# Kernel tuning notes

Measured on AMD Instinct MI355X. Metric: run time of the kernel, lower is better.

The kernel has to match this reference:

```python
import jax, jax.numpy as jnp
import numpy as np

C_M = 256   # norm_channel (msa channel)
C_Z = 128   # pair_channel
H = 8       # num_head
C = 32      # attention_channel per head


def layer_norm(x, gamma, beta, eps=1e-5):
    mu = jnp.mean(x, axis=-1, keepdims=True)
    var = jnp.var(x, axis=-1, keepdims=True)
    return (x - mu) * jax.lax.rsqrt(var + eps) * gamma + beta


def setup_inputs() -> dict:
    key = jax.random.key(0)
    ks = jax.random.split(key, 12)
    B, S, R = 1, 128, 256
    inp = {
        "msa_act": jax.random.normal(ks[0], (B, S, R, C_M), jnp.float32),
        "pair_act": jax.random.normal(ks[1], (B, R, R, C_Z), jnp.float32),
        "msa_mask": jnp.ones((B, S, R), jnp.float32),
        # query_norm params
        "qn_g": jnp.ones((C_M,), jnp.float32),
        "qn_b": jnp.zeros((C_M,), jnp.float32),
        # feat_2d_norm params
        "pn_g": jnp.ones((C_Z,), jnp.float32),
        "pn_b": jnp.zeros((C_Z,), jnp.float32),
        # feat_2d_weights: Linear(C_Z -> H, bias=False)
        "w2d": jax.random.normal(ks[2], (C_Z, H), jnp.float32) / np.sqrt(C_Z),
        # attention projections [C_M, H, C]
        "wq": jax.random.normal(ks[3], (C_M, H, C), jnp.float32) / np.sqrt(C_M),
        "wk": jax.random.normal(ks[4], (C_M, H, C), jnp.float32) / np.sqrt(C_M),
        "wv": jax.random.normal(ks[5], (C_M, H, C), jnp.float32) / np.sqrt(C_M),
        # gating linear [C_M, H, C] + bias
        "wg": jax.random.normal(ks[6], (C_M, H, C), jnp.float32) / np.sqrt(C_M),
        "bg": jnp.ones((H, C), jnp.float32),
        # output linear [H, C, C_M] + bias
        "wo": jax.random.normal(ks[7], (H, C, C_M), jnp.float32) / np.sqrt(H * C),
        "bo": jnp.zeros((C_M,), jnp.float32),
    }
    return inp


def reference(msa_act, pair_act, msa_mask, qn_g, qn_b, pn_g, pn_b, w2d,
              wq, wk, wv, wg, bg, wo, bo):
    # Pair bias: LayerNorm -> Linear(C_Z->H) -> permute to [B, 1, H, R, R]
    z = layer_norm(pair_act, pn_g, pn_b)            # [B, R, R, C_Z]
    z = jnp.einsum('bqkc,ch->bhqk', z, w2d)          # [B, H, R, R]
    z = z[:, None]                                   # [B, 1, H, R, R]

    # Mask bias: [B, S, 1, 1, R]
    mask_bias = (1e9 * (msa_mask - 1.0))[:, :, None, None, :]

    # Row-wise MHA with query norm
    m = layer_norm(msa_act, qn_g, qn_b)              # [B, S, R, C_M]
    scale = 1.0 / np.sqrt(C)
    q = jnp.einsum('bsqc,chd->bshqd', m, wq) * scale
    k = jnp.einsum('bskc,chd->bshkd', m, wk)
    v = jnp.einsum('bskc,chd->bshkd', m, wv)

    logits = jnp.einsum('bshqd,bshkd->bshqk', q, k) + mask_bias + z
    a = jax.nn.softmax(logits, axis=-1)              # [B, S, H, R, R]
    o = jnp.einsum('bshqk,bshkd->bsqhd', a, v)       # [B, S, R, H, C]

    g = jax.nn.sigmoid(jnp.einsum('bsqc,chd->bsqhd', m, wg) + bg)
    o = o * g
    out = jnp.einsum('bsqhd,hdc->bsqc', o, wo) + bo  # [B, S, R, C_M]
    return out
```

## Files before the change

kernel.cpp:

```cpp
#include <hip/hip_runtime.h>

typedef unsigned short u16;
typedef __attribute__((ext_vector_type(8))) short bf16x8;
typedef __attribute__((ext_vector_type(4))) float f32x4;

__device__ __forceinline__ float bf2f(u16 u){
  union { unsigned int i; float f; } v; v.i = ((unsigned int)u) << 16; return v.f;
}
__device__ __forceinline__ u16 f2bf(float f){
  union { float f; unsigned int i; } v; v.f = f;
  unsigned int i = v.i;
  return (u16)((i + 0x7fffu + ((i >> 16) & 1u)) >> 16);
}
__device__ __forceinline__ float ldin(const void* p, int i, int f){
  return f ? ((const float*)p)[i] : bf2f(((const u16*)p)[i]);
}
__device__ __forceinline__ void ld8(const void* p, int idx, int flag, float* out){
  if (flag) {
    const float* q = (const float*)p + idx;
    float4 a = *(const float4*)q, b = *(const float4*)(q + 4);
    out[0]=a.x; out[1]=a.y; out[2]=a.z; out[3]=a.w;
    out[4]=b.x; out[5]=b.y; out[6]=b.z; out[7]=b.w;
  } else {
    const u16* q = (const u16*)p + idx;
    uint4 u = *(const uint4*)q;
    const u16* h = (const u16*)&u;
    #pragma unroll
    for (int j = 0; j < 8; ++j) out[j] = bf2f(h[j]);
  }
}
__device__ __forceinline__ void gload16(const u16* g, u16* l){
  __builtin_amdgcn_global_load_lds(
      (const __attribute__((address_space(1))) void*)g,
      (__attribute__((address_space(3))) void*)l, 16, 0, 0);
}

__global__ void k_sniff(const unsigned int* __restrict__ msa_w, int* __restrict__ flag)
{
  int lane = threadIdx.x & 63;
  int lo0 = 0, expok = 0;
  #pragma unroll
  for (int j = 0; j < 4; ++j) {
    unsigned int w = msa_w[lane * 4 + j];
    if ((w & 0xffffu) == 0u) lo0++;
    unsigned int e = (w >> 7) & 0xffu;
    if (e >= 110u && e <= 140u) expok++;
  }
  #pragma unroll
  for (int off = 1; off < 64; off <<= 1) {
    lo0   += __shfl_xor(lo0,   off, 64);
    expok += __shfl_xor(expok, off, 64);
  }
  if (lane == 0 && blockIdx.x == 0)
    *flag = (lo0 > 200) ? 1 : ((expok > 200) ? 0 : 1);
}

__global__ __launch_bounds__(256) void k_transpose(
    const void* __restrict__ wq, const void* __restrict__ wk,
    const void* __restrict__ wv, const void* __restrict__ wg,
    const void* __restrict__ wo, const int* __restrict__ flagp,
    u16* __restrict__ Wt, u16* __restrict__ wot)
{
  const int flag = *flagp;
  int idx = blockIdx.x * 256 + threadIdx.x;
  int mat = idx >> 16;
  int col = (idx >> 8) & 255;
  int c   = idx & 255;
  const void* src = (mat == 0) ? wq : (mat == 1) ? wk : (mat == 2) ? wv
                  : (mat == 3) ? wg : wo;
  u16 v = f2bf(ldin(src, c * 256 + col, flag));
  if (idx < 262144) Wt[idx] = v;
  else              wot[idx - 262144] = v;
}

__global__ __launch_bounds__(256) void k_pair_z(
    const void* __restrict__ pair, const void* __restrict__ png,
    const void* __restrict__ pnb, const void* __restrict__ w2d,
    const int* __restrict__ flagp, float* __restrict__ z)
{
  const int flag = *flagp;
  const int t = threadIdx.x, lane = t & 63, wave = t >> 6;
  const int sub = lane >> 4, l15 = lane & 15;
  const int row = blockIdx.x * 16 + wave * 4 + sub;
  const int c0 = l15 * 8;
  float x[8];
  ld8(pair, row * 128 + c0, flag, x);
  float s = 0.f, sq = 0.f;
  #pragma unroll
  for (int j = 0; j < 8; ++j) { s += x[j]; sq += x[j] * x[j]; }
  #pragma unroll
  for (int off = 1; off < 16; off <<= 1) {
    s  += __shfl_xor(s,  off, 64);
    sq += __shfl_xor(sq, off, 64);
  }
  float mu = s * (1.f / 128.f);
  float var = sq * (1.f / 128.f) - mu * mu;
  float rs = rsqrtf(var + 1e-5f);
  float n[8];
  #pragma unroll
  for (int j = 0; j < 8; ++j)
    n[j] = (x[j] - mu) * rs * ldin(png, c0 + j, flag) + ldin(pnb, c0 + j, flag);
  float part[8] = {0.f,0.f,0.f,0.f,0.f,0.f,0.f,0.f};
  #pragma unroll
  for (int j = 0; j < 8; ++j) {
    float w[8];
    ld8(w2d, (c0 + j) * 8, flag, w);
    #pragma unroll
    for (int h = 0; h < 8; ++h) part[h] += n[j] * w[h];
  }
  #pragma unroll
  for (int h = 0; h < 8; ++h)
    #pragma unroll
    for (int off = 1; off < 16; off <<= 1)
      part[h] += __shfl_xor(part[h], off, 64);
  if (l15 < 8) {
    float outv = part[0];
    #pragma unroll
    for (int h = 1; h < 8; ++h) if (l15 == h) outv = part[h];
    z[l15 * 65536 + row] = outv;
  }
}

__global__ __launch_bounds__(256) void k_msa_ln(
    const void* __restrict__ msa, const void* __restrict__ qng,
    const void* __restrict__ qnb, const int* __restrict__ flagp,
    u16* __restrict__ m_bf)
{
  const int flag = *flagp;
  int wave = threadIdx.x >> 6, lane = threadIdx.x & 63;
  int row = blockIdx.x * 4 + wave;
  float x[4];
  if (flag) {
    float4 f4 = *((const float4*)msa + row * 64 + lane);
    x[0]=f4.x; x[1]=f4.y; x[2]=f4.z; x[3]=f4.w;
  } else {
    uint2 u = *((const uint2*)msa + row * 64 + lane);
    const u16* h = (const u16*)&u;
    #pragma unroll
    for (int j = 0; j < 4; ++j) x[j] = bf2f(h[j]);
  }
  float s = 0.f, sq = 0.f;
  #pragma unroll
  for (int j = 0; j < 4; ++j) { s += x[j]; sq += x[j] * x[j]; }
  #pragma unroll
  for (int off = 1; off < 64; off <<= 1) {
    s  += __shfl_xor(s,  off, 64);
    sq += __shfl_xor(sq, off, 64);
  }
  float mu = s * (1.f / 256.f);
  float var = sq * (1.f / 256.f) - mu * mu;
  float rs = rsqrtf(var + 1e-5f);
  u16 o[4];
  #pragma unroll
  for (int j = 0; j < 4; ++j) {
    int c = lane * 4 + j;
    o[j] = f2bf((x[j] - mu) * rs * ldin(qng, c, flag) + ldin(qnb, c, flag));
  }
  *((uint2*)m_bf + row * 64 + lane) = *(const uint2*)o;
}

__global__ __launch_bounds__(256) void k_qkvg(
    const u16* __restrict__ m_bf, const u16* __restrict__ Wt,
    const void* __restrict__ bg, const int* __restrict__ flagp,
    u16* __restrict__ q_ws, u16* __restrict__ k_ws,
    u16* __restrict__ v_ws, u16* __restrict__ g_ws)
{
  __shared__ u16 As[128 * 32];
  __shared__ u16 Bs[128 * 32];
  const int flag = *flagp;
  const int t = threadIdx.x, lane = t & 63, wave = t >> 6;
  const int wm = (wave >> 1) * 64, wn = (wave & 1) * 64;
  const int rowBase = blockIdx.x * 128;
  const int colBase = blockIdx.y * 128;
  const int g = lane >> 4, l15 = lane & 15;
  const int srow = wave * 32 + (lane >> 2);
  const int scol = (lane & 3) * 8;
  const u16* gA = m_bf + (rowBase + srow) * 256 + scol;
  const u16* gB = Wt   + (colBase + srow) * 256 + scol;
  u16* lA = As + wave * 32 * 32;
  u16* lB = Bs + wave * 32 * 32;

  f32x4 acc[4][4];
  f32x4 zero = {0.f, 0.f, 0.f, 0.f};
  #pragma unroll
  for (int i = 0; i < 4; ++i)
    #pragma unroll
    for (int j = 0; j < 4; ++j) acc[i][j] = zero;

  for (int kb = 0; kb < 256; kb += 32) {
    __syncthreads();
    gload16(gA + kb,            lA);
    gload16(gA + kb + 16 * 256, lA + 16 * 32);
    gload16(gB + kb,            lB);
    gload16(gB + kb + 16 * 256, lB + 16 * 32);
    __syncthreads();
    bf16x8 a[4], b[4];
    #pragma unroll
    for (int mt = 0; mt < 4; ++mt)
      a[mt] = *(const bf16x8*)(As + (wm + mt * 16 + l15) * 32 + g * 8);
    #pragma unroll
    for (int nt = 0; nt < 4; ++nt)
      b[nt] = *(const bf16x8*)(Bs + (wn + nt * 16 + l15) * 32 + g * 8);
    #pragma unroll
    for (int mt = 0; mt < 4; ++mt)
      #pragma unroll
      for (int nt = 0; nt < 4; ++nt)
        acc[mt][nt] = __builtin_amdgcn_mfma_f32_16x16x32_bf16(a[mt], b[nt], acc[mt][nt], 0, 0, 0);
  }

  const int t4 = colBase >> 8;
  const float scale = 0.17677669529663687f;
  #pragma unroll
  for (int mt = 0; mt < 4; ++mt)
    #pragma unroll
    for (int nt = 0; nt < 4; ++nt)
      #pragma unroll
      for (int r = 0; r < 4; ++r) {
        int row = rowBase + wm + mt * 16 + g * 4 + r;
        int col = colBase + wn + nt * 16 + l15;
        int s_ = row >> 8, ii = row & 255;
        int inner = col & 255, hh = inner >> 5, dd = inner & 31;
        float v = acc[mt][nt][r];
        if (t4 == 0)      q_ws[((s_ * 8 + hh) * 256 + ii) * 32 + dd] = f2bf(v * scale);
        else if (t4 == 1) k_ws[((s_ * 8 + hh) * 256 + ii) * 32 + dd] = f2bf(v);
        else if (t4 == 2) v_ws[((s_ * 8 + hh) * 256 + ii) * 32 + dd] = f2bf(v);
        else {
          float gv = v + ldin(bg, inner, flag);
          gv = 1.0f / (1.0f + __expf(-gv));
          g_ws[row * 256 + inner] = f2bf(gv);
        }
      }
}

__global__ __launch_bounds__(256) void k_attn(
    const u16* __restrict__ q_ws, const u16* __restrict__ k_ws,
    const u16* __restrict__ v_ws, const float* __restrict__ z,
    const void* __restrict__ mask, const u16* __restrict__ g_ws,
    const int* __restrict__ flagp, u16* __restrict__ og_ws)
{
  __shared__ u16 Ks[256 * 32];
  __shared__ u16 Vts[32 * 264];
  __shared__ u16 Pb[4 * 16 * 40];
  const int flag = *flagp;
  const int t = threadIdx.x, lane = t & 63, wave = t >> 6;
  const int sh = blockIdx.x;
  const int s_ = sh >> 3, h = sh & 7;

  {
    const uint4* srcK = (const uint4*)(k_ws + sh * 8192);
    uint4* dstK = (uint4*)Ks;
    #pragma unroll
    for (int j = 0; j < 4; ++j) dstK[t + 256 * j] = srcK[t + 256 * j];
    const u16* sv = v_ws + sh * 8192 + t * 32;
    uint4 v0 = *(const uint4*)sv, v1 = *(const uint4*)(sv + 8);
    const u16* ve = (const u16*)&v0;
    const u16* vo = (const u16*)&v1;
    #pragma unroll
    for (int d = 0; d < 8; ++d) Vts[d * 264 + t] = ve[d];
    #pragma unroll
    for (int d = 0; d < 8; ++d) Vts[(8 + d) * 264 + t] = vo[d];
    const u16* sv2 = sv + 16;
    uint4 v2 = *(const uint4*)sv2, v3 = *(const uint4*)(sv2 + 8);
    const u16* ve2 = (const u16*)&v2;
    const u16* vo2 = (const u16*)&v3;
    #pragma unroll
    for (int d = 0; d < 8; ++d) Vts[(16 + d) * 264 + t] = ve2[d];
    #pragma unroll
    for (int d = 0; d < 8; ++d) Vts[(24 + d) * 264 + t] = vo2[d];
  }
  __syncthreads();

  const int g = lane >> 4, l15 = lane & 15;
  const u16* qb = q_ws + sh * 8192;
  u16* pb = Pb + wave * 640;
  f32x4 zero = {0.f, 0.f, 0.f, 0.f};

  for (int qt = 0; qt < 4; ++qt) {
    const int qbase = wave * 64 + qt * 16;
    bf16x8 aq = *(const bf16x8*)(qb + (qbase + l15) * 32 + g * 8);
    f32x4 S[16];
    #pragma unroll
    for (int kt = 0; kt < 16; ++kt) {
      bf16x8 bk = *(const bf16x8*)(Ks + (kt * 16 + l15) * 32 + g * 8);
      S[kt] = __builtin_amdgcn_mfma_f32_16x16x32_bf16(aq, bk, zero, 0, 0, 0);
    }
    float mx[4] = {-1e30f, -1e30f, -1e30f, -1e30f};
    #pragma unroll
    for (int kt = 0; kt < 16; ++kt) {
      int k = kt * 16 + l15;
      float mb = 1e9f * (ldin(mask, s_ * 256 + k, flag) - 1.0f);
      const float* zp = z + h * 65536 + (qbase + g * 4) * 256 + k;
      #pragma unroll
      for (int r = 0; r < 4; ++r) {
        float val = S[kt][r] + mb + zp[r * 256];
        S[kt][r] = val;
        mx[r] = fmaxf(mx[r], val);
      }
    }
    #pragma unroll
    for (int r = 0; r < 4; ++r)
      #pragma unroll
      for (int off = 1; off < 16; off <<= 1)
        mx[r] = fmaxf(mx[r], __shfl_xor(mx[r], off, 64));
    float sm[4] = {0.f, 0.f, 0.f, 0.f};
    #pragma unroll
    for (int kt = 0; kt < 16; ++kt)
      #pragma unroll
      for (int r = 0; r < 4; ++r) {
        float p = __expf(S[kt][r] - mx[r]);
        S[kt][r] = p;
        sm[r] += p;
      }
    #pragma unroll
    for (int r = 0; r < 4; ++r)
      #pragma unroll
      for (int off = 1; off < 16; off <<= 1)
        sm[r] += __shfl_xor(sm[r], off, 64);

    f32x4 O0 = zero, O1 = zero;
    #pragma unroll
    for (int kc = 0; kc < 8; ++kc) {
      asm volatile("s_waitcnt lgkmcnt(0)" ::: "memory");
      #pragma unroll
      for (int half = 0; half < 2; ++half) {
        int kt = kc * 2 + half;
        #pragma unroll
        for (int r = 0; r < 4; ++r)
          pb[(g * 4 + r) * 40 + half * 16 + l15] = f2bf(S[kt][r]);
      }
      asm volatile("s_waitcnt lgkmcnt(0)" ::: "memory");
      bf16x8 ap  = *(const bf16x8*)(pb + l15 * 40 + g * 8);
      bf16x8 bv0 = *(const bf16x8*)(Vts + l15 * 264 + kc * 32 + g * 8);
      bf16x8 bv1 = *(const bf16x8*)(Vts + (16 + l15) * 264 + kc * 32 + g * 8);
      O0 = __builtin_amdgcn_mfma_f32_16x16x32_bf16(ap, bv0, O0, 0, 0, 0);
      O1 = __builtin_amdgcn_mfma_f32_16x16x32_bf16(ap, bv1, O1, 0, 0, 0);
    }
    #pragma unroll
    for (int r = 0; r < 4; ++r) {
      float inv = 1.0f / sm[r];
      int qq = qbase + g * 4 + r;
      int base = (s_ * 256 + qq) * 256 + h * 32;
      float o0 = O0[r] * inv * bf2f(g_ws[base + l15]);
      float o1 = O1[r] * inv * bf2f(g_ws[base + 16 + l15]);
      og_ws[base + l15]      = f2bf(o0);
      og_ws[base + 16 + l15] = f2bf(o1);
    }
  }
}

__global__ __launch_bounds__(256) void k_outproj(
    const u16* __restrict__ og, const u16* __restrict__ wot,
    const void* __restrict__ bo, const int* __restrict__ flagp,
    void* __restrict__ outv)
{
  __shared__ u16 As[128 * 32];
  __shared__ u16 Bs[128 * 32];
  const int flag = *flagp;
  const int t = threadIdx.x, lane = t & 63, wave = t >> 6;
  const int wm = (wave >> 1) * 64, wn = (wave & 1) * 64;
  const int rowBase = blockIdx.x * 128;
  const int colBase = blockIdx.y * 128;
  const int g = lane >> 4, l15 = lane & 15;
  const int srow = wave * 32 + (lane >> 2);
  const int scol = (lane & 3) * 8;
  const u16* gA = og  + (rowBase + srow) * 256 + scol;
  const u16* gB = wot + (colBase + srow) * 256 + scol;
  u16* lA = As + wave * 32 * 32;
  u16* lB = Bs + wave * 32 * 32;

  f32x4 acc[4][4];
  f32x4 zero = {0.f, 0.f, 0.f, 0.f};
  #pragma unroll
  for (int i = 0; i < 4; ++i)
    #pragma unroll
    for (int j = 0; j < 4; ++j) acc[i][j] = zero;

  for (int kb = 0; kb < 256; kb += 32) {
    __syncthreads();
    gload16(gA + kb,            lA);
    gload16(gA + kb + 16 * 256, lA + 16 * 32);
    gload16(gB + kb,            lB);
    gload16(gB + kb + 16 * 256, lB + 16 * 32);
    __syncthreads();
    bf16x8 a[4], b[4];
    #pragma unroll
    for (int mt = 0; mt < 4; ++mt)
      a[mt] = *(const bf16x8*)(As + (wm + mt * 16 + l15) * 32 + g * 8);
    #pragma unroll
    for (int nt = 0; nt < 4; ++nt)
      b[nt] = *(const bf16x8*)(Bs + (wn + nt * 16 + l15) * 32 + g * 8);
    #pragma unroll
    for (int mt = 0; mt < 4; ++mt)
      #pragma unroll
      for (int nt = 0; nt < 4; ++nt)
        acc[mt][nt] = __builtin_amdgcn_mfma_f32_16x16x32_bf16(a[mt], b[nt], acc[mt][nt], 0, 0, 0);
  }
  #pragma unroll
  for (int mt = 0; mt < 4; ++mt)
    #pragma unroll
    for (int nt = 0; nt < 4; ++nt)
      #pragma unroll
      for (int r = 0; r < 4; ++r) {
        int row = rowBase + wm + mt * 16 + g * 4 + r;
        int col = colBase + wn + nt * 16 + l15;
        float val = acc[mt][nt][r] + ldin(bo, col, flag);
        if (flag) ((float*)outv)[row * 256 + col] = val;
        else      ((u16*)outv)[row * 256 + col]   = f2bf(val);
      }
}

extern "C" void kernel_launch(void* const* d_in, const int* in_sizes, int n_in,
                              void* d_out, int out_size, void* d_ws, size_t ws_size,
                              hipStream_t stream)
{
  const void* msa  = d_in[0];
  const void* pair = d_in[1];
  const void* mask = d_in[2];
  const void* qng  = d_in[3];
  const void* qnb  = d_in[4];
  const void* png  = d_in[5];
  const void* pnb  = d_in[6];
  const void* w2d  = d_in[7];
  const void* wq   = d_in[8];
  const void* wk   = d_in[9];
  const void* wv   = d_in[10];
  const void* wg   = d_in[11];
  const void* bg   = d_in[12];
  const void* wo   = d_in[13];
  const void* bo   = d_in[14];

  char* ws = (char*)d_ws;
  float* z   = (float*)(ws + 0);
  u16* Wt    = (u16*)(ws + 2097152);
  u16* wot   = (u16*)(ws + 2621440);
  int* flag  = (int*)(ws + 2752512);
  u16* m_bf  = (u16*)(ws + 2752768);
  u16* og_ws = m_bf;
  u16* q_ws  = (u16*)(ws + 19529984);
  u16* k_ws  = (u16*)(ws + 36307200);
  u16* v_ws  = (u16*)(ws + 53084416);
  u16* g_ws  = (u16*)(ws + 69861632);

  hipLaunchKernelGGL(k_sniff, dim3(1), dim3(64), 0, stream,
                     (const unsigned int*)msa, flag);
  hipLaunchKernelGGL(k_transpose, dim3(1280), dim3(256), 0, stream,
                     wq, wk, wv, wg, wo, flag, Wt, wot);
  hipLaunchKernelGGL(k_pair_z, dim3(4096), dim3(256), 0, stream,
                     pair, png, pnb, w2d, flag, z);
  hipLaunchKernelGGL(k_msa_ln, dim3(8192), dim3(256), 0, stream,
                     msa, qng, qnb, flag, m_bf);
  hipLaunchKernelGGL(k_qkvg, dim3(256, 8), dim3(256), 0, stream,
                     m_bf, Wt, bg, flag, q_ws, k_ws, v_ws, g_ws);
  hipLaunchKernelGGL(k_attn, dim3(1024), dim3(256), 0, stream,
                     q_ws, k_ws, v_ws, z, mask, g_ws, flag, og_ws);
  hipLaunchKernelGGL(k_outproj, dim3(256, 2), dim3(256), 0, stream,
                     og_ws, wot, bo, flag, d_out);
}
```

Measured before the change: 312.6 us.

## Use MFMA for pair bias, stage QKVG epilogue via LDS, transpose softmax rows

The pair-bias kernel now layer-normalizes 64 rows per block into LDS and computes the C_Z->H projection with bf16 MFMA instead of per-thread FMAs and shuffle reductions. The QKVG GEMM epilogue stages tiles in shared memory so q/k/v/g are written with coalesced 16-byte stores. The attention softmax transposes the score tile through LDS so each lane holds contiguous keys of one query row, reads z and the mask as float4 vectors, and reduces across fewer lanes. It also packs probabilities to bf16 in registers and moves the pair kernel launch after qkvg. The trade-offs are bf16 rounding of the normalized pair activations and more LDS traffic and synchronization.

```diff
diff --git a/kernel.cpp b/kernel.cpp
--- a/kernel.cpp
+++ b/kernel.cpp
@@ -15,19 +15,11 @@
 __device__ __forceinline__ float ldin(const void* p, int i, int f){
   return f ? ((const float*)p)[i] : bf2f(((const u16*)p)[i]);
 }
-__device__ __forceinline__ void ld8(const void* p, int idx, int flag, float* out){
-  if (flag) {
-    const float* q = (const float*)p + idx;
-    float4 a = *(const float4*)q, b = *(const float4*)(q + 4);
-    out[0]=a.x; out[1]=a.y; out[2]=a.z; out[3]=a.w;
-    out[4]=b.x; out[5]=b.y; out[6]=b.z; out[7]=b.w;
-  } else {
-    const u16* q = (const u16*)p + idx;
-    uint4 u = *(const uint4*)q;
-    const u16* h = (const u16*)&u;
-    #pragma unroll
-    for (int j = 0; j < 8; ++j) out[j] = bf2f(h[j]);
-  }
+__device__ __forceinline__ bf16x8 pack8(const float* v){
+  union { bf16x8 v8; u16 h[8]; } u;
+  #pragma unroll
+  for (int j = 0; j < 8; ++j) u.h[j] = f2bf(v[j]);
+  return u.v8;
 }
 __device__ __forceinline__ void gload16(const u16* g, u16* l){
   __builtin_amdgcn_global_load_lds(
@@ -78,46 +70,71 @@
     const void* __restrict__ pnb, const void* __restrict__ w2d,
     const int* __restrict__ flagp, float* __restrict__ z)
 {
+  __shared__ u16 As[64 * 136];
+  __shared__ u16 Bs[16 * 136];
   const int flag = *flagp;
   const int t = threadIdx.x, lane = t & 63, wave = t >> 6;
-  const int sub = lane >> 4, l15 = lane & 15;
-  const int row = blockIdx.x * 16 + wave * 4 + sub;
-  const int c0 = l15 * 8;
-  float x[8];
-  ld8(pair, row * 128 + c0, flag, x);
-  float s = 0.f, sq = 0.f;
-  #pragma unroll
-  for (int j = 0; j < 8; ++j) { s += x[j]; sq += x[j] * x[j]; }
-  #pragma unroll
-  for (int off = 1; off < 16; off <<= 1) {
-    s  += __shfl_xor(s,  off, 64);
-    sq += __shfl_xor(sq, off, 64);
-  }
-  float mu = s * (1.f / 128.f);
-  float var = sq * (1.f / 128.f) - mu * mu;
-  float rs = rsqrtf(var + 1e-5f);
-  float n[8];
-  #pragma unroll
-  for (int j = 0; j < 8; ++j)
-    n[j] = (x[j] - mu) * rs * ldin(png, c0 + j, flag) + ldin(pnb, c0 + j, flag);
-  float part[8] = {0.f,0.f,0.f,0.f,0.f,0.f,0.f,0.f};
-  #pragma unroll
-  for (int j = 0; j < 8; ++j) {
-    float w[8];
-    ld8(w2d, (c0 + j) * 8, flag, w);
-    #pragma unroll
-    for (int h = 0; h < 8; ++h) part[h] += n[j] * w[h];
-  }
-  #pragma unroll
-  for (int h = 0; h < 8; ++h)
-    #pragma unroll
-    for (int off = 1; off < 16; off <<= 1)
-      part[h] += __shfl_xor(part[h], off, 64);
+  const int g = lane >> 4, l15 = lane & 15;
+  const int rowBase = blockIdx.x * 64;
+
+  if (t < 128) {
+    #pragma unroll
+    for (int n = 0; n < 16; ++n)
+      Bs[n * 136 + t] = (n < 8) ? f2bf(ldin(w2d, t * 8 + n, flag)) : (u16)0;
+  }
+  {
+    int lrow = t >> 2, cb = (t & 3) * 32;
+    int base = (rowBase + lrow) * 128 + cb;
+    float x[32];
+    if (flag) {
+      const float* p = (const float*)pair + base;
+      #pragma unroll
+      for (int j = 0; j < 8; ++j) {
+        float4 f4 = *(const float4*)(p + 4 * j);
+        x[4*j] = f4.x; x[4*j+1] = f4.y; x[4*j+2] = f4.z; x[4*j+3] = f4.w;
+      }
+    } else {
+      const u16* p = (const u16*)pair + base;
+      #pragma unroll
+      for (int j = 0; j < 4; ++j) {
+        uint4 u = *(const uint4*)(p + 8 * j);
+        const u16* h = (const u16*)&u;
+        #pragma unroll
+        for (int e = 0; e < 8; ++e) x[8*j+e] = bf2f(h[e]);
+      }
+    }
+    float s = 0.f, sq = 0.f;
+    #pragma unroll
+    for (int j = 0; j < 32; ++j) { s += x[j]; sq += x[j] * x[j]; }
+    s  += __shfl_xor(s, 1, 64);  s  += __shfl_xor(s, 2, 64);
+    sq += __shfl_xor(sq, 1, 64); sq += __shfl_xor(sq, 2, 64);
+    float mu = s * (1.f / 128.f);
+    float var = sq * (1.f / 128.f) - mu * mu;
+    float rs = rsqrtf(var + 1e-5f);
+    u16 o[32];
+    #pragma unroll
+    for (int j = 0; j < 32; ++j) {
+      int c = cb + j;
+      o[j] = f2bf((x[j] - mu) * rs * ldin(png, c, flag) + ldin(pnb, c, flag));
+    }
+    u16* dst = As + lrow * 136 + cb;
+    #pragma unroll
+    for (int j = 0; j < 4; ++j)
+      *(uint4*)(dst + 8 * j) = *(const uint4*)(o + 8 * j);
+  }
+  __syncthreads();
+
+  f32x4 accz = {0.f, 0.f, 0.f, 0.f};
+  #pragma unroll
+  for (int kb = 0; kb < 4; ++kb) {
+    bf16x8 a = *(const bf16x8*)(As + (wave * 16 + l15) * 136 + kb * 32 + g * 8);
+    bf16x8 b = *(const bf16x8*)(Bs + l15 * 136 + kb * 32 + g * 8);
+    accz = __builtin_amdgcn_mfma_f32_16x16x32_bf16(a, b, accz, 0, 0, 0);
+  }
   if (l15 < 8) {
-    float outv = part[0];
-    #pragma unroll
-    for (int h = 1; h < 8; ++h) if (l15 == h) outv = part[h];
-    z[l15 * 65536 + row] = outv;
+    #pragma unroll
+    for (int r = 0; r < 4; ++r)
+      z[l15 * 65536 + rowBase + wave * 16 + g * 4 + r] = accz[r];
   }
 }
 
@@ -165,8 +182,9 @@
     u16* __restrict__ q_ws, u16* __restrict__ k_ws,
     u16* __restrict__ v_ws, u16* __restrict__ g_ws)
 {
-  __shared__ u16 As[128 * 32];
-  __shared__ u16 Bs[128 * 32];
+  __shared__ u16 SM[64 * 136];
+  u16* As = SM;
+  u16* Bs = SM + 4096;
   const int flag = *flagp;
   const int t = threadIdx.x, lane = t & 63, wave = t >> 6;
   const int wm = (wave >> 1) * 64, wn = (wave & 1) * 64;
@@ -210,26 +228,51 @@
 
   const int t4 = colBase >> 8;
   const float scale = 0.17677669529663687f;
-  #pragma unroll
-  for (int mt = 0; mt < 4; ++mt)
-    #pragma unroll
-    for (int nt = 0; nt < 4; ++nt)
-      #pragma unroll
-      for (int r = 0; r < 4; ++r) {
-        int row = rowBase + wm + mt * 16 + g * 4 + r;
-        int col = colBase + wn + nt * 16 + l15;
-        int s_ = row >> 8, ii = row & 255;
-        int inner = col & 255, hh = inner >> 5, dd = inner & 31;
-        float v = acc[mt][nt][r];
-        if (t4 == 0)      q_ws[((s_ * 8 + hh) * 256 + ii) * 32 + dd] = f2bf(v * scale);
-        else if (t4 == 1) k_ws[((s_ * 8 + hh) * 256 + ii) * 32 + dd] = f2bf(v);
-        else if (t4 == 2) v_ws[((s_ * 8 + hh) * 256 + ii) * 32 + dd] = f2bf(v);
-        else {
-          float gv = v + ldin(bg, inner, flag);
-          gv = 1.0f / (1.0f + __expf(-gv));
-          g_ws[row * 256 + inner] = f2bf(gv);
-        }
+  const int hbase = (colBase >> 5) & 7;
+  const int s_ = rowBase >> 8;
+  #pragma unroll
+  for (int p = 0; p < 2; ++p) {
+    __syncthreads();
+    if ((wave >> 1) == p) {
+      #pragma unroll
+      for (int mt = 0; mt < 4; ++mt)
+        #pragma unroll
+        for (int nt = 0; nt < 4; ++nt)
+          #pragma unroll
+          for (int r = 0; r < 4; ++r) {
+            int rr = mt * 16 + g * 4 + r;
+            int cc = wn + nt * 16 + l15;
+            float v = acc[mt][nt][r];
+            u16 o;
+            if (t4 == 0) o = f2bf(v * scale);
+            else if (t4 == 3) {
+              float gv = v + ldin(bg, (colBase & 255) + cc, flag);
+              o = f2bf(1.0f / (1.0f + __expf(-gv)));
+            } else o = f2bf(v);
+            SM[rr * 136 + cc] = o;
+          }
+    }
+    __syncthreads();
+    int iibase = (rowBase & 255) + p * 64;
+    if (t4 < 3) {
+      u16* dst_ws = (t4 == 0) ? q_ws : (t4 == 1) ? k_ws : v_ws;
+      int rr = t >> 2, dseg = t & 3;
+      #pragma unroll
+      for (int hl = 0; hl < 4; ++hl) {
+        uint4 vd = *(const uint4*)(SM + rr * 136 + hl * 32 + dseg * 8);
+        *(uint4*)(dst_ws + ((s_ * 8 + hbase + hl) * 256 + iibase + rr) * 32 + dseg * 8) = vd;
       }
+    } else {
+      int cbase = colBase & 255;
+      int rr4 = t >> 4, cseg = t & 15;
+      #pragma unroll
+      for (int jr = 0; jr < 4; ++jr) {
+        int rr = jr * 16 + rr4;
+        uint4 vd = *(const uint4*)(SM + rr * 136 + cseg * 8);
+        *(uint4*)(g_ws + (s_ * 256 + iibase + rr) * 256 + cbase + cseg * 8) = vd;
+      }
+    }
+  }
 }
 
 __global__ __launch_bounds__(256) void k_attn(
@@ -240,7 +283,8 @@
 {
   __shared__ u16 Ks[256 * 32];
   __shared__ u16 Vts[32 * 264];
-  __shared__ u16 Pb[4 * 16 * 40];
+  __shared__ float Tb[4][16 * 36];
+  __shared__ float Mb[256];
   const int flag = *flagp;
   const int t = threadIdx.x, lane = t & 63, wave = t >> 6;
   const int sh = blockIdx.x;
@@ -267,12 +311,13 @@
     for (int d = 0; d < 8; ++d) Vts[(16 + d) * 264 + t] = ve2[d];
     #pragma unroll
     for (int d = 0; d < 8; ++d) Vts[(24 + d) * 264 + t] = vo2[d];
+    Mb[t] = 1e9f * (ldin(mask, s_ * 256 + t, flag) - 1.0f);
   }
   __syncthreads();
 
   const int g = lane >> 4, l15 = lane & 15;
   const u16* qb = q_ws + sh * 8192;
-  u16* pb = Pb + wave * 640;
+  float* Tw = &Tb[wave][0];
   f32x4 zero = {0.f, 0.f, 0.f, 0.f};
 
   for (int qt = 0; qt < 4; ++qt) {
@@ -284,52 +329,50 @@
       bf16x8 bk = *(const bf16x8*)(Ks + (kt * 16 + l15) * 32 + g * 8);
       S[kt] = __builtin_amdgcn_mfma_f32_16x16x32_bf16(aq, bk, zero, 0, 0, 0);
     }
-    float mx[4] = {-1e30f, -1e30f, -1e30f, -1e30f};
-    #pragma unroll
-    for (int kt = 0; kt < 16; ++kt) {
-      int k = kt * 16 + l15;
-      float mb = 1e9f * (ldin(mask, s_ * 256 + k, flag) - 1.0f);
-      const float* zp = z + h * 65536 + (qbase + g * 4) * 256 + k;
-      #pragma unroll
-      for (int r = 0; r < 4; ++r) {
-        float val = S[kt][r] + mb + zp[r * 256];
-        S[kt][r] = val;
-        mx[r] = fmaxf(mx[r], val);
-      }
-    }
-    #pragma unroll
-    for (int r = 0; r < 4; ++r)
-      #pragma unroll
-      for (int off = 1; off < 16; off <<= 1)
-        mx[r] = fmaxf(mx[r], __shfl_xor(mx[r], off, 64));
-    float sm[4] = {0.f, 0.f, 0.f, 0.f};
-    #pragma unroll
-    for (int kt = 0; kt < 16; ++kt)
-      #pragma unroll
-      for (int r = 0; r < 4; ++r) {
-        float p = __expf(S[kt][r] - mx[r]);
-        S[kt][r] = p;
-        sm[r] += p;
-      }
-    #pragma unroll
-    for (int r = 0; r < 4; ++r)
-      #pragma unroll
-      for (int off = 1; off < 16; off <<= 1)
-        sm[r] += __shfl_xor(sm[r], off, 64);
-
-    f32x4 O0 = zero, O1 = zero;
+    float L[8][8];
+    const float* zr = z + h * 65536 + (qbase + l15) * 256;
     #pragma unroll
     for (int kc = 0; kc < 8; ++kc) {
       asm volatile("s_waitcnt lgkmcnt(0)" ::: "memory");
       #pragma unroll
-      for (int half = 0; half < 2; ++half) {
-        int kt = kc * 2 + half;
+      for (int half = 0; half < 2; ++half)
         #pragma unroll
         for (int r = 0; r < 4; ++r)
-          pb[(g * 4 + r) * 40 + half * 16 + l15] = f2bf(S[kt][r]);
+          Tw[(g * 4 + r) * 36 + half * 16 + l15] = S[kc * 2 + half][r];
+      asm volatile("s_waitcnt lgkmcnt(0)" ::: "memory");
+      float4 t0 = *(const float4*)(Tw + l15 * 36 + g * 8);
+      float4 t1 = *(const float4*)(Tw + l15 * 36 + g * 8 + 4);
+      float4 m0 = *(const float4*)(Mb + kc * 32 + g * 8);
+      float4 m1 = *(const float4*)(Mb + kc * 32 + g * 8 + 4);
+      float4 z0 = *(const float4*)(zr + kc * 32 + g * 8);
+      float4 z1 = *(const float4*)(zr + kc * 32 + g * 8 + 4);
+      L[kc][0] = t0.x + m0.x + z0.x;  L[kc][1] = t0.y + m0.y + z0.y;
+      L[kc][2] = t0.z + m0.z + z0.z;  L[kc][3] = t0.w + m0.w + z0.w;
+      L[kc][4] = t1.x + m1.x + z1.x;  L[kc][5] = t1.y + m1.y + z1.y;
+      L[kc][6] = t1.z + m1.z + z1.z;  L[kc][7] = t1.w + m1.w + z1.w;
+    }
+    float mx = -1e30f;
+    #pragma unroll
+    for (int kc = 0; kc < 8; ++kc)
+      #pragma unroll
+      for (int j = 0; j < 8; ++j) mx = fmaxf(mx, L[kc][j]);
+    mx = fmaxf(mx, __shfl_xor(mx, 16, 64));
+    mx = fmaxf(mx, __shfl_xor(mx, 32, 64));
+    float sm = 0.f;
+    #pragma unroll
+    for (int kc = 0; kc < 8; ++kc)
+      #pragma unroll
+      for (int j = 0; j < 8; ++j) {
+        float p = __expf(L[kc][j] - mx);
+        L[kc][j] = p;
+        sm += p;
       }
-      asm volatile("s_waitcnt lgkmcnt(0)" ::: "memory");
-      bf16x8 ap  = *(const bf16x8*)(pb + l15 * 40 + g * 8);
+    sm += __shfl_xor(sm, 16, 64);
+    sm += __shfl_xor(sm, 32, 64);
+    f32x4 O0 = zero, O1 = zero;
+    #pragma unroll
+    for (int kc = 0; kc < 8; ++kc) {
+      bf16x8 ap  = pack8(&L[kc][0]);
       bf16x8 bv0 = *(const bf16x8*)(Vts + l15 * 264 + kc * 32 + g * 8);
       bf16x8 bv1 = *(const bf16x8*)(Vts + (16 + l15) * 264 + kc * 32 + g * 8);
       O0 = __builtin_amdgcn_mfma_f32_16x16x32_bf16(ap, bv0, O0, 0, 0, 0);
@@ -337,7 +380,8 @@
     }
     #pragma unroll
     for (int r = 0; r < 4; ++r) {
-      float inv = 1.0f / sm[r];
+      float smr = __shfl(sm, g * 4 + r, 64);
+      float inv = 1.0f / smr;
       int qq = qbase + g * 4 + r;
       int base = (s_ * 256 + qq) * 256 + h * 32;
       float o0 = O0[r] * inv * bf2f(g_ws[base + l15]);
@@ -445,12 +489,12 @@
                      (const unsigned int*)msa, flag);
   hipLaunchKernelGGL(k_transpose, dim3(1280), dim3(256), 0, stream,
                      wq, wk, wv, wg, wo, flag, Wt, wot);
-  hipLaunchKernelGGL(k_pair_z, dim3(4096), dim3(256), 0, stream,
-                     pair, png, pnb, w2d, flag, z);
   hipLaunchKernelGGL(k_msa_ln, dim3(8192), dim3(256), 0, stream,
                      msa, qng, qnb, flag, m_bf);
   hipLaunchKernelGGL(k_qkvg, dim3(256, 8), dim3(256), 0, stream,
                      m_bf, Wt, bg, flag, q_ws, k_ws, v_ws, g_ws);
+  hipLaunchKernelGGL(k_pair_z, dim3(1024), dim3(256), 0, stream,
+                     pair, png, pnb, w2d, flag, z);
   hipLaunchKernelGGL(k_attn, dim3(1024), dim3(256), 0, stream,
                      q_ws, k_ws, v_ws, z, mask, g_ws, flag, og_ws);
   hipLaunchKernelGGL(k_outproj, dim3(256, 2), dim3(256), 0, stream,
```

Result: faster. 303.3 us (-3.0%).
